# Optimization experiments

Hardware: AMD Instinct MI355X
Metric: run time of the kernel (lower is better)

Reference implementation:

```python
import jax, jax.numpy as jnp
import numpy as np
from jax import lax


def T_grid(t, num_coeff):
    # Chebyshev polynomials T_0..T_{N-1} evaluated at t -> (N, len(t))
    rows = [jnp.ones_like(t), t]
    for _ in range(2, num_coeff):
        rows.append(2.0 * t * rows[-1] - rows[-2])
    return jnp.stack(rows[:num_coeff], axis=0)


def setup_inputs() -> dict:
    key = jax.random.key(0)
    k1, k2, k3, k4, k5 = jax.random.split(key, 5)
    B, D, H, N, T = 128, 512, 1024, 32, 16
    return {
        "t_span": jnp.linspace(0.0, 1.0, T, dtype=jnp.float32),
        "y_init": jax.random.normal(k1, (B, D), dtype=jnp.float32),
        "B_init": jax.random.uniform(k2, (B, D, N), dtype=jnp.float32),
        "W1": jax.random.normal(k3, (D, H), dtype=jnp.float32) / jnp.sqrt(jnp.float32(D)),
        "b1": jax.random.normal(k4, (H,), dtype=jnp.float32),
        "W2": jax.random.normal(k5, (H, D), dtype=jnp.float32) / jnp.sqrt(jnp.float32(H)),
        "num_coeff_per_dim": 32,
        "max_iters": 10,
    }


def reference(t_span, y_init, B_init, W1, b1, W2, num_coeff_per_dim, max_iters):
    N = num_coeff_per_dim
    t0, t1 = t_span[0], t_span[-1]

    # Chebyshev-Gauss-Lobatto nodes on [-1, 1] and Simpson midpoints interleaved
    t_cheb = -jnp.cos(jnp.pi * (jnp.arange(N, dtype=t_span.dtype) / (N - 1)))  # (N,)
    mids = 0.5 * (t_cheb[1:] + t_cheb[:-1])
    t_simpsons = jnp.zeros(2 * N - 1, dtype=t_span.dtype).at[::2].set(t_cheb).at[1::2].set(mids)
    t_true = t0 + 0.5 * (t1 - t0) * (t_simpsons + 1.0)  # (2N-1,)

    Phi_f = T_grid(t_simpsons, N)        # (N, 2N-1)
    Phi = Phi_f[:, ::2]                  # (N, N), invert ONCE (reused every iter)
    Phi_inv = jnp.linalg.inv(Phi)
    widths = (t_true[2::2] - t_true[:-2:2]) / 6.0  # (N-1,) Simpson interval weights

    def f_all(Y):  # vector field f(t, y) = tanh(y @ W1 + t*b1) @ W2, all nodes at once
        # Y: (B, D, M) with M = 2N-1
        h = jnp.tanh(jnp.einsum("bdm,dh->bhm", Y, W1) + t_true[None, None, :] * b1[None, :, None])
        return jnp.einsum("bhm,hd->bdm", h, W2)

    def step(Bc, _):
        approx = jnp.einsum("bdn,nm->bdm", Bc, Phi_f)          # (B, D, 2N-1)
        fap = f_all(approx)
        # Simpson's rule per Chebyshev interval, then cumulative integral S
        s = widths * (fap[..., :-2:2] + 4.0 * fap[..., 1:-1:2] + fap[..., 2::2])  # (B,D,N-1)
        S = jnp.concatenate([jnp.zeros_like(s[..., :1]), jnp.cumsum(s, axis=-1)], axis=-1)
        # torch.linalg.solve(Phi, S + y0, left=False): Bn @ Phi = S + y0
        Bn = (S + y_init[..., None]) @ Phi_inv
        return Bn, None

    B_final, _ = lax.scan(step, B_init, None, length=max_iters)

    t_out = -1.0 + 2.0 * (t_span - t0) / (t1 - t0)
    Phi_out = T_grid(t_out, N)                                  # (N, T)
    approx = jnp.einsum("bdn,nt->bdt", B_final, Phi_out)        # (B, D, T)
    return jnp.moveaxis(approx, -1, 0), B_final                 # (T, B, D), (B, D, N)
```

## Files before the change

### kernel.cpp

```cpp
#include <hip/hip_runtime.h>
#include <hip/hip_bf16.h>
#include <math.h>

#define BB 128
#define DD 512
#define HH 1024
#define NB 32
#define MM 63
#define TT 16
#define ITERS 10

#define OFF_U       0
#define OFF_TTRUE   64
#define OFF_PHIOUT  128
#define OFF_PHIF_BF 1024
#define OFF_QT_BF   2048
#define HDRF        4096
#define OFF_PTPA    HDRF
#define OFF_PTP0    (OFF_PTPA + 2097152)
#define OFF_W1P     (OFF_PTP0 + 2097152)
#define OFF_W2P     (OFF_W1P + 262144)
#define OFF_WWP     (OFF_W2P + 262144)
#define OFF_YW1     (OFF_WWP + 524288)

typedef __attribute__((ext_vector_type(8))) short bf16x8;
typedef __attribute__((ext_vector_type(4))) float f32x4;

static __device__ __forceinline__ unsigned short f2bf(float f) {
    unsigned int x = __builtin_bit_cast(unsigned int, f);
    unsigned int r = x + 0x7FFFu + ((x >> 16) & 1u);
    return (unsigned short)(r >> 16);
}

static __device__ __forceinline__ void store4bf(unsigned short* p,
                                                float v0, float v1, float v2, float v3) {
    unsigned int lo = (unsigned int)f2bf(v0) | ((unsigned int)f2bf(v1) << 16);
    unsigned int hi = (unsigned int)f2bf(v2) | ((unsigned int)f2bf(v3) << 16);
    uint2 u; u.x = lo; u.y = hi;
    *(uint2*)p = u;
}

static __device__ __forceinline__ float tanh_fast(float x) {
    float e = exp2f(x * 2.88539008177793f);
    return 1.0f - 2.0f / (e + 1.0f);
}

static __device__ __forceinline__ unsigned short* aS(unsigned short* smA, int r, int c16) {
    return (unsigned short*)((char*)smA + (((r << 10) + (c16 << 4)) ^ ((r & 7) << 4)));
}

__global__ __launch_bounds__(256) void prologue_kernel(
        const float* __restrict__ t_span, const float* __restrict__ W1,
        const float* __restrict__ W2, const float* __restrict__ y_init,
        float* __restrict__ ws) {
    __shared__ __align__(16) char smem[66560];
    const int bid  = blockIdx.x;
    const int t    = threadIdx.x;
    const int lane = t & 63;
    const int w    = t >> 6;
    const int q    = lane >> 4;
    const int l15  = lane & 15;

    if (bid == 0) {
        double* tsim    = (double*)(smem + 0);
        double* ttrue_d = (double*)(smem + 512);
        double* wid     = (double*)(smem + 1024);
        double* phid    = (double*)(smem + 1280);
        double* pinv    = (double*)(smem + 17408);
        double* Rl      = (double*)(smem + 34048);
        double* Qd      = (double*)(smem + 50176);

        const double PI = 3.14159265358979323846;
        const double t0 = (double)t_span[0];
        const double t1 = (double)t_span[TT - 1];

        if (t < MM) {
            double v;
            if ((t & 1) == 0) {
                int j = t >> 1;
                v = -cos(PI * (double)j / (double)(NB - 1));
            } else {
                int i = t >> 1;
                double a = -cos(PI * (double)i / (double)(NB - 1));
                double b = -cos(PI * (double)(i + 1) / (double)(NB - 1));
                v = 0.5 * (a + b);
            }
            tsim[t] = v;
            ttrue_d[t] = t0 + 0.5 * (t1 - t0) * (v + 1.0);
        }
        __syncthreads();
        if (t < 31) wid[t] = (ttrue_d[2 * t + 2] - ttrue_d[2 * t]) / 6.0;
        if (t < MM) ws[OFF_TTRUE + t] = (float)ttrue_d[t];
        if (t == 63) ws[OFF_TTRUE + 63] = 0.0f;

        if (t < MM) {
            double x = tsim[t];
            double r0 = 1.0, r1 = x;
            phid[0 * MM + t] = r0;
            phid[1 * MM + t] = r1;
            for (int n = 2; n < NB; n++) {
                double r2 = 2.0 * x * r1 - r0;
                phid[n * MM + t] = r2;
                r0 = r1; r1 = r2;
            }
        }

        for (int f = t; f < NB * NB; f += 256) {
            int i = f >> 5, j = f & 31;
            double ci = (i == 0 || i == NB - 1) ? 2.0 : 1.0;
            double cj = (j == 0 || j == NB - 1) ? 2.0 : 1.0;
            double v = 2.0 * cos(PI * (double)(i * j) / (double)(NB - 1))
                       / ((double)(NB - 1) * ci * cj);
            pinv[f] = (j & 1) ? -v : v;
        }
        __syncthreads();

        {
            unsigned short* pf = (unsigned short*)(ws + OFF_PHIF_BF);
            for (int f = t; f < 64 * 32; f += 256) {
                int m = f >> 5, n = f & 31;
                pf[f] = f2bf(m < MM ? (float)phid[n * MM + m] : 0.0f);
            }
        }

        if (t < MM) {
            double acc = 0.0;
            Rl[t * NB + 0] = 0.0;
            for (int i = 1; i < NB; i++) {
                int ip = i - 1;
                double wv = 0.0;
                if (t == 2 * ip)     wv += wid[ip];
                if (t == 2 * ip + 1) wv += 4.0 * wid[ip];
                if (t == 2 * ip + 2) wv += wid[ip];
                acc += wv;
                Rl[t * NB + i] = acc;
            }
        }
        __syncthreads();

        for (int f = t; f < MM * NB; f += 256) {
            int m = f >> 5, j = f & 31;
            double s = 0.0;
            for (int i = 0; i < NB; i++) s += Rl[m * NB + i] * pinv[i * 32 + j];
            Qd[f] = s;
        }
        __syncthreads();

        {
            unsigned short* qt = (unsigned short*)(ws + OFF_QT_BF);
            for (int f = t; f < 32 * 64; f += 256) {
                int j = f >> 6, m = f & 63;
                qt[f] = f2bf(m < MM ? (float)Qd[m * NB + j] : 0.0f);
            }
        }
        if (t < NB) {
            double s = 0.0;
            for (int i = 0; i < NB; i++) s += pinv[i * 32 + t];
            ws[OFF_U + t] = (float)s;
        }
        if (t < TT) {
            double x = -1.0 + 2.0 * ((double)t_span[t] - t0) / (t1 - t0);
            double r0 = 1.0, r1 = x;
            ws[OFF_PHIOUT + 0 * TT + t] = 1.0f;
            ws[OFF_PHIOUT + 1 * TT + t] = (float)x;
            for (int n = 2; n < NB; n++) {
                double r2 = 2.0 * x * r1 - r0;
                ws[OFF_PHIOUT + n * TT + t] = (float)r2;
                r0 = r1; r1 = r2;
            }
        }
        return;
    }

    if (bid <= 64) {
        unsigned short* W1p = (unsigned short*)(ws + OFF_W1P);
        const int hb = bid - 1;
        #pragma unroll
        for (int i = 0; i < 4; i++) {
            int f = i * 256 + t;
            int ds = f >> 6, ln = f & 63;
            int qq = ln >> 4, ll = ln & 15;
            unsigned short tmp[8];
            #pragma unroll
            for (int e = 0; e < 8; e++)
                tmp[e] = f2bf(W1[(size_t)(ds * 32 + qq * 8 + e) * HH + hb * 16 + ll]);
            *(uint4*)(W1p + ((size_t)(hb * 16 + ds) * 64 + ln) * 8) = *(uint4*)tmp;
        }
        return;
    }

    if (bid <= 96) {
        unsigned short* W2p = (unsigned short*)(ws + OFF_W2P);
        const int db = bid - 65;
        #pragma unroll
        for (int i = 0; i < 8; i++) {
            int f = i * 256 + t;
            int hs = f >> 6, ln = f & 63;
            int qq = ln >> 4, ll = ln & 15;
            unsigned short tmp[8];
            #pragma unroll
            for (int e = 0; e < 8; e++)
                tmp[e] = f2bf(W2[(size_t)(hs * 32 + qq * 8 + e) * DD + db * 16 + ll]);
            *(uint4*)(W2p + ((size_t)(db * 32 + hs) * 64 + ln) * 8) = *(uint4*)tmp;
        }
        return;
    }

    unsigned short* lw1t = (unsigned short*)smem;

    if (bid <= 352) {
        unsigned short* WWp = (unsigned short*)(ws + OFF_WWP);
        unsigned short* pbounce = (unsigned short*)(smem + 33280);
        const int idx   = bid - 97;
        const int h2grp = idx & 31;
        const int hpb   = (idx >> 5) * 4 + w;
        const int h2c0  = h2grp * 32;

        for (int i = 0; i < 64; i++) {
            int f = i * 256 + t;
            int row = f >> 5, col = f & 31;
            lw1t[col * 520 + row] = f2bf(W1[(size_t)row * HH + h2c0 + col]);
        }
        __syncthreads();

        f32x4 acc[2][2] = {};
        #pragma unroll 4
        for (int ds = 0; ds < 16; ds++) {
            bf16x8 a[2];
            #pragma unroll
            for (int mt = 0; mt < 2; mt++) {
                const float* w2r = W2 + (size_t)(hpb * 32 + mt * 16 + l15) * DD + ds * 32 + q * 8;
                float4 va = *(const float4*)w2r;
                float4 vb = *(const float4*)(w2r + 4);
                unsigned short tmp[8] = { f2bf(va.x), f2bf(va.y), f2bf(va.z), f2bf(va.w),
                                          f2bf(vb.x), f2bf(vb.y), f2bf(vb.z), f2bf(vb.w) };
                a[mt] = *(bf16x8*)tmp;
            }
            bf16x8 bb0 = *(const bf16x8*)(lw1t + l15 * 520 + ds * 32 + q * 8);
            bf16x8 bb1 = *(const bf16x8*)(lw1t + (16 + l15) * 520 + ds * 32 + q * 8);
            acc[0][0] = __builtin_amdgcn_mfma_f32_16x16x32_bf16(a[0], bb0, acc[0][0], 0, 0, 0);
            acc[0][1] = __builtin_amdgcn_mfma_f32_16x16x32_bf16(a[0], bb1, acc[0][1], 0, 0, 0);
            acc[1][0] = __builtin_amdgcn_mfma_f32_16x16x32_bf16(a[1], bb0, acc[1][0], 0, 0, 0);
            acc[1][1] = __builtin_amdgcn_mfma_f32_16x16x32_bf16(a[1], bb1, acc[1][1], 0, 0, 0);
        }
        unsigned short* pb = pbounce + w * 1024;
        #pragma unroll
        for (int mt = 0; mt < 2; mt++)
            #pragma unroll
            for (int nt = 0; nt < 2; nt++) {
                int lane8 = (mt * 2 + (q >> 1)) * 16 + l15;
                #pragma unroll
                for (int r = 0; r < 4; r++)
                    pb[(nt * 64 + lane8) * 8 + (q & 1) * 4 + r] = f2bf(acc[mt][nt][r]);
            }
        uint4 f0 = *(uint4*)(pb + (0 * 64 + lane) * 8);
        uint4 f1 = *(uint4*)(pb + (1 * 64 + lane) * 8);
        int h2b0 = h2grp * 2;
        *(uint4*)(WWp + ((size_t)(h2b0 + 0) * 32 + hpb) * 512 + lane * 8) = f0;
        *(uint4*)(WWp + ((size_t)(h2b0 + 1) * 32 + hpb) * 512 + lane * 8) = f1;
        return;
    }

    {
        float* yW1 = ws + OFF_YW1;
        const int h2grp = bid - 353;
        const int h2c0  = h2grp * 32;

        for (int i = 0; i < 64; i++) {
            int f = i * 256 + t;
            int row = f >> 5, col = f & 31;
            lw1t[col * 520 + row] = f2bf(W1[(size_t)row * HH + h2c0 + col]);
        }
        __syncthreads();

        f32x4 acc[2][2] = {};
        #pragma unroll 4
        for (int ds = 0; ds < 16; ds++) {
            bf16x8 a[2];
            #pragma unroll
            for (int mt = 0; mt < 2; mt++) {
                const float* yr = y_init + (size_t)(w * 32 + mt * 16 + l15) * DD + ds * 32 + q * 8;
                float4 va = *(const float4*)yr;
                float4 vb = *(const float4*)(yr + 4);
                unsigned short tmp[8] = { f2bf(va.x), f2bf(va.y), f2bf(va.z), f2bf(va.w),
                                          f2bf(vb.x), f2bf(vb.y), f2bf(vb.z), f2bf(vb.w) };
                a[mt] = *(bf16x8*)tmp;
            }
            bf16x8 bb0 = *(const bf16x8*)(lw1t + l15 * 520 + ds * 32 + q * 8);
            bf16x8 bb1 = *(const bf16x8*)(lw1t + (16 + l15) * 520 + ds * 32 + q * 8);
            acc[0][0] = __builtin_amdgcn_mfma_f32_16x16x32_bf16(a[0], bb0, acc[0][0], 0, 0, 0);
            acc[0][1] = __builtin_amdgcn_mfma_f32_16x16x32_bf16(a[0], bb1, acc[0][1], 0, 0, 0);
            acc[1][0] = __builtin_amdgcn_mfma_f32_16x16x32_bf16(a[1], bb0, acc[1][0], 0, 0, 0);
            acc[1][1] = __builtin_amdgcn_mfma_f32_16x16x32_bf16(a[1], bb1, acc[1][1], 0, 0, 0);
        }
        #pragma unroll
        for (int mt = 0; mt < 2; mt++)
            #pragma unroll
            for (int nt = 0; nt < 2; nt++)
                #pragma unroll
                for (int r = 0; r < 4; r++) {
                    int b  = w * 32 + mt * 16 + q * 4 + r;
                    int h2 = h2c0 + nt * 16 + l15;
                    yW1[(size_t)b * HH + h2] = acc[mt][nt][r];
                }
    }
}

__global__ __launch_bounds__(256) void k1_kernel(
        const float* __restrict__ B_init,
        const unsigned short* __restrict__ W1p,
        const float* __restrict__ b1,
        const float* __restrict__ ws,
        unsigned short* __restrict__ Ptp)
{
    __shared__ __align__(16) char smem[40960];
    unsigned short* smA  = (unsigned short*)smem;
    unsigned short* t_sb = (unsigned short*)smem;
    unsigned short* g_sb = (unsigned short*)(smem + 32768);

    const int t    = threadIdx.x;
    const int lane = t & 63;
    const int w    = t >> 6;
    const int q    = lane >> 4;
    const int l15  = lane & 15;
    const int bid  = blockIdx.x;
    const int b    = bid & 127;
    const int hblk = bid >> 7;
    const int hw   = hblk * 128 + w * 32;

    {
        const float* Bi = B_init + (size_t)b * DD * NB;
        #pragma unroll 8
        for (int i = 0; i < 64; i++) {
            int f = i * 256 + t;
            int d = f >> 5, n = f & 31;
            *(unsigned short*)(smem + (((n << 10) + (d << 1)) ^ ((n & 7) << 4)))
                = f2bf(Bi[f]);
        }
    }
    __syncthreads();

    f32x4 acc[2][2] = {};
    const unsigned short* W1b = W1p + (size_t)(hw >> 4) * 8192;
    #pragma unroll 4
    for (int d0 = 0; d0 < DD; d0 += 32) {
        int c16 = (d0 >> 3) + q;
        int ds  = d0 >> 5;
        bf16x8 a0  = *(const bf16x8*)aS(smA, l15, c16);
        bf16x8 a1  = *(const bf16x8*)aS(smA, 16 + l15, c16);
        bf16x8 bb0 = *(const bf16x8*)(W1b + ds * 512 + lane * 8);
        bf16x8 bb1 = *(const bf16x8*)(W1b + 8192 + ds * 512 + lane * 8);
        acc[0][0] = __builtin_amdgcn_mfma_f32_16x16x32_bf16(a0, bb0, acc[0][0], 0, 0, 0);
        acc[0][1] = __builtin_amdgcn_mfma_f32_16x16x32_bf16(a0, bb1, acc[0][1], 0, 0, 0);
        acc[1][0] = __builtin_amdgcn_mfma_f32_16x16x32_bf16(a1, bb0, acc[1][0], 0, 0, 0);
        acc[1][1] = __builtin_amdgcn_mfma_f32_16x16x32_bf16(a1, bb1, acc[1][1], 0, 0, 0);
    }
    #pragma unroll
    for (int mt = 0; mt < 2; mt++)
        #pragma unroll
        for (int nt = 0; nt < 2; nt++) {
            int hl = w * 32 + nt * 16 + l15;
            store4bf(&g_sb[hl * 32 + mt * 16 + q * 4],
                     acc[mt][nt][0], acc[mt][nt][1], acc[mt][nt][2], acc[mt][nt][3]);
        }
    __syncthreads();

    f32x4 zacc[4][2] = {};
    const unsigned short* PF = (const unsigned short*)(ws + OFF_PHIF_BF);
    bf16x8 gb[2];
    #pragma unroll
    for (int nt = 0; nt < 2; nt++)
        gb[nt] = *(const bf16x8*)(&g_sb[(w * 32 + nt * 16 + l15) * 32 + q * 8]);
    #pragma unroll
    for (int mt = 0; mt < 4; mt++) {
        bf16x8 af = *(const bf16x8*)(PF + (mt * 16 + l15) * 32 + q * 8);
        zacc[mt][0] = __builtin_amdgcn_mfma_f32_16x16x32_bf16(af, gb[0], zacc[mt][0], 0, 0, 0);
        zacc[mt][1] = __builtin_amdgcn_mfma_f32_16x16x32_bf16(af, gb[1], zacc[mt][1], 0, 0, 0);
    }

    const float* TTp = ws + OFF_TTRUE;
    float b1v[2] = { b1[hw + l15], b1[hw + 16 + l15] };
    #pragma unroll
    for (int mt = 0; mt < 4; mt++) {
        float4 ttv = *(const float4*)(TTp + mt * 16 + q * 4);
        #pragma unroll
        for (int nt = 0; nt < 2; nt++) {
            int hl = w * 32 + nt * 16 + l15;
            float v0 = tanh_fast(zacc[mt][nt][0] + ttv.x * b1v[nt]);
            float v1 = tanh_fast(zacc[mt][nt][1] + ttv.y * b1v[nt]);
            float v2 = tanh_fast(zacc[mt][nt][2] + ttv.z * b1v[nt]);
            float v3 = tanh_fast(zacc[mt][nt][3] + ttv.w * b1v[nt]);
            store4bf(&t_sb[hl * 72 + mt * 16 + q * 4], v0, v1, v2, v3);
        }
    }
    __syncthreads();

    f32x4 pacc[2][2] = {};
    const unsigned short* QT = (const unsigned short*)(ws + OFF_QT_BF);
    #pragma unroll
    for (int ks = 0; ks < 2; ks++) {
        bf16x8 bt[2];
        #pragma unroll
        for (int nt = 0; nt < 2; nt++)
            bt[nt] = *(const bf16x8*)(&t_sb[(w * 32 + nt * 16 + l15) * 72 + ks * 32 + q * 8]);
        #pragma unroll
        for (int jt = 0; jt < 2; jt++) {
            bf16x8 aq = *(const bf16x8*)(QT + (jt * 16 + l15) * 64 + ks * 32 + q * 8);
            pacc[jt][0] = __builtin_amdgcn_mfma_f32_16x16x32_bf16(aq, bt[0], pacc[jt][0], 0, 0, 0);
            pacc[jt][1] = __builtin_amdgcn_mfma_f32_16x16x32_bf16(aq, bt[1], pacc[jt][1], 0, 0, 0);
        }
    }

    {
        unsigned short* pb = g_sb + w * 1024;
        #pragma unroll
        for (int jt = 0; jt < 2; jt++)
            #pragma unroll
            for (int nt = 0; nt < 2; nt++) {
                int grp = (nt * 2 + (l15 >> 3)) & 3;
                #pragma unroll
                for (int r = 0; r < 4; r++) {
                    int lane8 = grp * 16 + q * 4 + r;
                    pb[(jt * 64 + lane8) * 8 + (l15 & 7)] = f2bf(pacc[jt][nt][r]);
                }
            }
        int hs = hblk * 4 + w;
        uint4 f0 = *(uint4*)(pb + (0 * 64 + lane) * 8);
        uint4 f1 = *(uint4*)(pb + (1 * 64 + lane) * 8);
        *(uint4*)(Ptp + (((size_t)(b * 32 + hs) * 2 + 0) * 64 + lane) * 8) = f0;
        *(uint4*)(Ptp + (((size_t)(b * 32 + hs) * 2 + 1) * 64 + lane) * 8) = f1;
    }
}

__global__ __launch_bounds__(256) void kf_kernel(
        const unsigned short* __restrict__ Ptin,
        const unsigned short* __restrict__ WWp,
        const float* __restrict__ yW1,
        const float* __restrict__ b1,
        const float* __restrict__ ws,
        unsigned short* __restrict__ Ptout)
{
    __shared__ __align__(16) char smem[69632];
    const int t    = threadIdx.x;
    const int lane = t & 63;
    const int w    = t >> 6;
    const int q    = lane >> 4;
    const int l15  = lane & 15;
    const int bid  = blockIdx.x;
    const int b    = bid & 127;
    const int hblk2 = bid >> 7;
    const int hw   = hblk2 * 256 + w * 64;

    f32x4 acc[2][4] = {};
    const unsigned short* Ab  = Ptin + (size_t)b * 32768;
    const unsigned short* WWb = WWp + (size_t)(hblk2 * 16 + w * 4) * 16384;
    unsigned short* buf0 = (unsigned short*)smem;
    unsigned short* buf1 = (unsigned short*)(smem + 16384);

    {
        const uint4* src = (const uint4*)Ab;
        uint4* dst = (uint4*)buf0;
        #pragma unroll
        for (int i = 0; i < 4; i++) dst[i * 256 + t] = src[i * 256 + t];
    }
    __syncthreads();

    #pragma unroll 1
    for (int c = 0; c < 4; ++c) {
        if (c < 3) {
            const uint4* src = (const uint4*)(Ab + (c + 1) * 8192);
            uint4* dst = (uint4*)((c & 1) ? buf0 : buf1);
            #pragma unroll
            for (int i = 0; i < 4; i++) dst[i * 256 + t] = src[i * 256 + t];
        }
        const unsigned short* Ac = (c & 1) ? buf1 : buf0;
        #pragma unroll
        for (int sl = 0; sl < 8; ++sl) {
            int s = c * 8 + sl;
            bf16x8 a0 = *(const bf16x8*)(Ac + (sl * 2 + 0) * 512 + lane * 8);
            bf16x8 a1 = *(const bf16x8*)(Ac + (sl * 2 + 1) * 512 + lane * 8);
            #pragma unroll
            for (int nt = 0; nt < 4; nt++) {
                bf16x8 bb = *(const bf16x8*)(WWb + nt * 16384 + s * 512 + lane * 8);
                acc[0][nt] = __builtin_amdgcn_mfma_f32_16x16x32_bf16(a0, bb, acc[0][nt], 0, 0, 0);
                acc[1][nt] = __builtin_amdgcn_mfma_f32_16x16x32_bf16(a1, bb, acc[1][nt], 0, 0, 0);
            }
        }
        __syncthreads();
    }

    unsigned short* g_w  = (unsigned short*)(smem + w * 4096);
    unsigned short* t_w  = (unsigned short*)(smem + 16384 + w * 9216);
    unsigned short* pb_w = (unsigned short*)(smem + 53248 + w * 4096);

    const float* U = ws + OFF_U;
    float yw[4];
    #pragma unroll
    for (int nt = 0; nt < 4; nt++)
        yw[nt] = yW1[(size_t)b * HH + hw + nt * 16 + l15];
    #pragma unroll
    for (int mt = 0; mt < 2; mt++) {
        float4 uv = *(const float4*)(U + mt * 16 + q * 4);
        #pragma unroll
        for (int nt = 0; nt < 4; nt++) {
            int hl = nt * 16 + l15;
            store4bf(&g_w[hl * 32 + mt * 16 + q * 4],
                     acc[mt][nt][0] + uv.x * yw[nt],
                     acc[mt][nt][1] + uv.y * yw[nt],
                     acc[mt][nt][2] + uv.z * yw[nt],
                     acc[mt][nt][3] + uv.w * yw[nt]);
        }
    }

    f32x4 zacc[4][4] = {};
    const unsigned short* PF = (const unsigned short*)(ws + OFF_PHIF_BF);
    bf16x8 gb[4];
    #pragma unroll
    for (int nt = 0; nt < 4; nt++)
        gb[nt] = *(const bf16x8*)(&g_w[(nt * 16 + l15) * 32 + q * 8]);
    #pragma unroll
    for (int mt = 0; mt < 4; mt++) {
        bf16x8 af = *(const bf16x8*)(PF + (mt * 16 + l15) * 32 + q * 8);
        #pragma unroll
        for (int nt = 0; nt < 4; nt++)
            zacc[mt][nt] = __builtin_amdgcn_mfma_f32_16x16x32_bf16(af, gb[nt], zacc[mt][nt], 0, 0, 0);
    }

    const float* TTp = ws + OFF_TTRUE;
    float b1v[4];
    #pragma unroll
    for (int nt = 0; nt < 4; nt++)
        b1v[nt] = b1[hw + nt * 16 + l15];
    #pragma unroll
    for (int mt = 0; mt < 4; mt++) {
        float4 ttv = *(const float4*)(TTp + mt * 16 + q * 4);
        #pragma unroll
        for (int nt = 0; nt < 4; nt++) {
            int hl = nt * 16 + l15;
            float v0 = tanh_fast(zacc[mt][nt][0] + ttv.x * b1v[nt]);
            float v1 = tanh_fast(zacc[mt][nt][1] + ttv.y * b1v[nt]);
            float v2 = tanh_fast(zacc[mt][nt][2] + ttv.z * b1v[nt]);
            float v3 = tanh_fast(zacc[mt][nt][3] + ttv.w * b1v[nt]);
            store4bf(&t_w[hl * 72 + mt * 16 + q * 4], v0, v1, v2, v3);
        }
    }

    f32x4 pacc[2][4] = {};
    const unsigned short* QT = (const unsigned short*)(ws + OFF_QT_BF);
    #pragma unroll
    for (int ks = 0; ks < 2; ks++) {
        bf16x8 bt[4];
        #pragma unroll
        for (int nt = 0; nt < 4; nt++)
            bt[nt] = *(const bf16x8*)(&t_w[(nt * 16 + l15) * 72 + ks * 32 + q * 8]);
        #pragma unroll
        for (int jt = 0; jt < 2; jt++) {
            bf16x8 aq = *(const bf16x8*)(QT + (jt * 16 + l15) * 64 + ks * 32 + q * 8);
            #pragma unroll
            for (int nt = 0; nt < 4; nt++)
                pacc[jt][nt] = __builtin_amdgcn_mfma_f32_16x16x32_bf16(aq, bt[nt], pacc[jt][nt], 0, 0, 0);
        }
    }

    {
        #pragma unroll
        for (int jt = 0; jt < 2; jt++)
            #pragma unroll
            for (int nt = 0; nt < 4; nt++) {
                int grp    = ((nt & 1) * 2 + (l15 >> 3)) & 3;
                int hs_loc = nt >> 1;
                #pragma unroll
                for (int r = 0; r < 4; r++) {
                    int lane8 = grp * 16 + q * 4 + r;
                    pb_w[(hs_loc * 2 + jt) * 512 + lane8 * 8 + (l15 & 7)] = f2bf(pacc[jt][nt][r]);
                }
            }
        int hs0 = hblk2 * 8 + w * 2;
        #pragma unroll
        for (int i = 0; i < 4; i++) {
            uint4 fv = *(uint4*)(pb_w + i * 512 + lane * 8);
            int hs = hs0 + (i >> 1), jt = i & 1;
            *(uint4*)(Ptout + (((size_t)(b * 32 + hs) * 2 + jt) * 64 + lane) * 8) = fv;
        }
    }
}

__global__ __launch_bounds__(256) void k2f_kernel(
        const unsigned short* __restrict__ Ptp,
        const unsigned short* __restrict__ W2p,
        const float* __restrict__ y_init,
        const float* __restrict__ ws,
        float* __restrict__ out)
{
    __shared__ __align__(16) float ls[4 * 544];
    __shared__ float phiout_s[NB * TT];

    const int t    = threadIdx.x;
    const int lane = t & 63;
    const int w    = t >> 6;
    const int q    = lane >> 4;
    const int l15  = lane & 15;
    const int bid  = blockIdx.x;
    const int b    = bid & 127;
    const int dblk = bid >> 7;
    const int dw   = dblk * 64 + w * 16;

    for (int f = t; f < NB * TT; f += 256) phiout_s[f] = ws[OFF_PHIOUT + f];

    f32x4 acc[2] = {};
    const unsigned short* Ab  = Ptp + (size_t)b * 32768;
    const unsigned short* W2b = W2p + (size_t)(dblk * 4 + w) * 16384;
    #pragma unroll 4
    for (int s = 0; s < 32; s++) {
        bf16x8 a0 = *(const bf16x8*)(Ab + (s * 2 + 0) * 512 + lane * 8);
        bf16x8 a1 = *(const bf16x8*)(Ab + (s * 2 + 1) * 512 + lane * 8);
        bf16x8 bb = *(const bf16x8*)(W2b + s * 512 + lane * 8);
        acc[0] = __builtin_amdgcn_mfma_f32_16x16x32_bf16(a0, bb, acc[0], 0, 0, 0);
        acc[1] = __builtin_amdgcn_mfma_f32_16x16x32_bf16(a1, bb, acc[1], 0, 0, 0);
    }

    const float* U = ws + OFF_U;
    float yv = y_init[(size_t)b * DD + dw + l15];
    #pragma unroll
    for (int mt = 0; mt < 2; mt++) {
        float4 uv = *(const float4*)(U + mt * 16 + q * 4);
        #pragma unroll
        for (int r = 0; r < 4; r++) {
            int j = mt * 16 + q * 4 + r;
            float uvr = (r == 0) ? uv.x : (r == 1) ? uv.y : (r == 2) ? uv.z : uv.w;
            ls[w * 544 + j * 17 + l15] = acc[mt][r] + yv * uvr;
        }
    }
    __syncthreads();

    float* out1 = out + (size_t)TT * BB * DD;
    #pragma unroll
    for (int it = 0; it < 8; it++) {
        int f = it * 64 + lane;
        int d_l = f >> 5, j2 = f & 31;
        out1[((size_t)b * DD + dw + d_l) * NB + j2] = ls[w * 544 + j2 * 17 + d_l];
    }

    #pragma unroll
    for (int i = 0; i < 4; i++) {
        int idx = i * 256 + t;
        int t16 = idx >> 6, dl = idx & 63;
        float s = 0.f;
        #pragma unroll
        for (int n = 0; n < NB; n++)
            s += ls[(dl >> 4) * 544 + n * 17 + (dl & 15)] * phiout_s[n * TT + t16];
        out[(size_t)t16 * (BB * DD) + (size_t)b * DD + dblk * 64 + dl] = s;
    }
}

extern "C" void kernel_launch(void* const* d_in, const int* in_sizes, int n_in,
                              void* d_out, int out_size, void* d_ws, size_t ws_size,
                              hipStream_t stream) {
    const float* t_span = (const float*)d_in[0];
    const float* y_init = (const float*)d_in[1];
    const float* B_init = (const float*)d_in[2];
    const float* W1     = (const float*)d_in[3];
    const float* b1     = (const float*)d_in[4];
    const float* W2     = (const float*)d_in[5];
    float* ws  = (float*)d_ws;
    float* out = (float*)d_out;

    unsigned short* W1p  = (unsigned short*)(ws + OFF_W1P);
    unsigned short* W2p  = (unsigned short*)(ws + OFF_W2P);
    unsigned short* WWp  = (unsigned short*)(ws + OFF_WWP);
    float*          yW1  = ws + OFF_YW1;
    unsigned short* PtpA = (unsigned short*)(ws + OFF_PTPA);
    unsigned short* PtpB = (unsigned short*)(ws + OFF_PTP0);

    prologue_kernel<<<dim3(385), 256, 0, stream>>>(t_span, W1, W2, y_init, ws);

    k1_kernel<<<dim3(1024), 256, 0, stream>>>(B_init, W1p, b1, ws, PtpA);

    unsigned short* pin  = PtpA;
    unsigned short* pout = PtpB;
    for (int it = 1; it < ITERS; it++) {
        kf_kernel<<<dim3(512), 256, 0, stream>>>(pin, WWp, yW1, b1, ws, pout);
        unsigned short* tmp = pin; pin = pout; pout = tmp;
    }
    k2f_kernel<<<dim3(1024), 256, 0, stream>>>(pin, W2p, y_init, ws, out);
}
```

Before: 338.4 us.

## Halve per-block H tile in kf_kernel and double grid to 1024 blocks

Each block of the fused iteration kernel now covers 128 hidden units instead of 256, with each wave handling 32 instead of 64. The grid grows from 512 to 1024 blocks, shared memory drops from 68 KB to 32 KB, and the accumulator arrays shrink. The aim is more parallelism and occupancy on the GPU's many CUs. In exchange, each block's A-tile (Ptin per batch row) is loaded from global memory twice as often, so there is less reuse per load.

```diff
diff --git a/kernel.cpp b/kernel.cpp
--- a/kernel.cpp
+++ b/kernel.cpp
@@ -440,7 +440,7 @@
         const float* __restrict__ ws,
         unsigned short* __restrict__ Ptout)
 {
-    __shared__ __align__(16) char smem[69632];
+    __shared__ __align__(16) char smem[32768];
     const int t    = threadIdx.x;
     const int lane = t & 63;
     const int w    = t >> 6;
@@ -448,12 +448,12 @@
     const int l15  = lane & 15;
     const int bid  = blockIdx.x;
     const int b    = bid & 127;
-    const int hblk2 = bid >> 7;
-    const int hw   = hblk2 * 256 + w * 64;
-
-    f32x4 acc[2][4] = {};
+    const int hblk = bid >> 7;
+    const int hw   = hblk * 128 + w * 32;
+
+    f32x4 acc[2][2] = {};
     const unsigned short* Ab  = Ptin + (size_t)b * 32768;
-    const unsigned short* WWb = WWp + (size_t)(hblk2 * 16 + w * 4) * 16384;
+    const unsigned short* WWb = WWp + (size_t)(hw >> 4) * 16384;
     unsigned short* buf0 = (unsigned short*)smem;
     unsigned short* buf1 = (unsigned short*)(smem + 16384);
 
@@ -477,32 +477,29 @@
         #pragma unroll
         for (int sl = 0; sl < 8; ++sl) {
             int s = c * 8 + sl;
-            bf16x8 a0 = *(const bf16x8*)(Ac + (sl * 2 + 0) * 512 + lane * 8);
-            bf16x8 a1 = *(const bf16x8*)(Ac + (sl * 2 + 1) * 512 + lane * 8);
-            #pragma unroll
-            for (int nt = 0; nt < 4; nt++) {
-                bf16x8 bb = *(const bf16x8*)(WWb + nt * 16384 + s * 512 + lane * 8);
-                acc[0][nt] = __builtin_amdgcn_mfma_f32_16x16x32_bf16(a0, bb, acc[0][nt], 0, 0, 0);
-                acc[1][nt] = __builtin_amdgcn_mfma_f32_16x16x32_bf16(a1, bb, acc[1][nt], 0, 0, 0);
-            }
+            bf16x8 a0  = *(const bf16x8*)(Ac + (sl * 2 + 0) * 512 + lane * 8);
+            bf16x8 a1  = *(const bf16x8*)(Ac + (sl * 2 + 1) * 512 + lane * 8);
+            bf16x8 bb0 = *(const bf16x8*)(WWb + s * 512 + lane * 8);
+            bf16x8 bb1 = *(const bf16x8*)(WWb + 16384 + s * 512 + lane * 8);
+            acc[0][0] = __builtin_amdgcn_mfma_f32_16x16x32_bf16(a0, bb0, acc[0][0], 0, 0, 0);
+            acc[0][1] = __builtin_amdgcn_mfma_f32_16x16x32_bf16(a0, bb1, acc[0][1], 0, 0, 0);
+            acc[1][0] = __builtin_amdgcn_mfma_f32_16x16x32_bf16(a1, bb0, acc[1][0], 0, 0, 0);
+            acc[1][1] = __builtin_amdgcn_mfma_f32_16x16x32_bf16(a1, bb1, acc[1][1], 0, 0, 0);
         }
         __syncthreads();
     }
-
-    unsigned short* g_w  = (unsigned short*)(smem + w * 4096);
-    unsigned short* t_w  = (unsigned short*)(smem + 16384 + w * 9216);
-    unsigned short* pb_w = (unsigned short*)(smem + 53248 + w * 4096);
+    unsigned short* g_w = (unsigned short*)(smem + w * 2048);
+    unsigned short* t_w = (unsigned short*)(smem + 8192 + w * 4608);
+    unsigned short* pb_w = g_w;
 
     const float* U = ws + OFF_U;
-    float yw[4];
-    #pragma unroll
-    for (int nt = 0; nt < 4; nt++)
-        yw[nt] = yW1[(size_t)b * HH + hw + nt * 16 + l15];
+    float yw[2] = { yW1[(size_t)b * HH + hw + l15],
+                    yW1[(size_t)b * HH + hw + 16 + l15] };
     #pragma unroll
     for (int mt = 0; mt < 2; mt++) {
         float4 uv = *(const float4*)(U + mt * 16 + q * 4);
         #pragma unroll
-        for (int nt = 0; nt < 4; nt++) {
+        for (int nt = 0; nt < 2; nt++) {
             int hl = nt * 16 + l15;
             store4bf(&g_w[hl * 32 + mt * 16 + q * 4],
                      acc[mt][nt][0] + uv.x * yw[nt],
@@ -512,30 +509,26 @@
         }
     }
 
-    f32x4 zacc[4][4] = {};
+    f32x4 zacc[4][2] = {};
     const unsigned short* PF = (const unsigned short*)(ws + OFF_PHIF_BF);
-    bf16x8 gb[4];
-    #pragma unroll
-    for (int nt = 0; nt < 4; nt++)
+    bf16x8 gb[2];
+    #pragma unroll
+    for (int nt = 0; nt < 2; nt++)
         gb[nt] = *(const bf16x8*)(&g_w[(nt * 16 + l15) * 32 + q * 8]);
     #pragma unroll
     for (int mt = 0; mt < 4; mt++) {
         bf16x8 af = *(const bf16x8*)(PF + (mt * 16 + l15) * 32 + q * 8);
-        #pragma unroll
-        for (int nt = 0; nt < 4; nt++)
-            zacc[mt][nt] = __builtin_amdgcn_mfma_f32_16x16x32_bf16(af, gb[nt], zacc[mt][nt], 0, 0, 0);
+        zacc[mt][0] = __builtin_amdgcn_mfma_f32_16x16x32_bf16(af, gb[0], zacc[mt][0], 0, 0, 0);
+        zacc[mt][1] = __builtin_amdgcn_mfma_f32_16x16x32_bf16(af, gb[1], zacc[mt][1], 0, 0, 0);
     }
 
     const float* TTp = ws + OFF_TTRUE;
-    float b1v[4];
-    #pragma unroll
-    for (int nt = 0; nt < 4; nt++)
-        b1v[nt] = b1[hw + nt * 16 + l15];
+    float b1v[2] = { b1[hw + l15], b1[hw + 16 + l15] };
     #pragma unroll
     for (int mt = 0; mt < 4; mt++) {
         float4 ttv = *(const float4*)(TTp + mt * 16 + q * 4);
         #pragma unroll
-        for (int nt = 0; nt < 4; nt++) {
+        for (int nt = 0; nt < 2; nt++) {
             int hl = nt * 16 + l15;
             float v0 = tanh_fast(zacc[mt][nt][0] + ttv.x * b1v[nt]);
             float v1 = tanh_fast(zacc[mt][nt][1] + ttv.y * b1v[nt]);
@@ -545,20 +538,19 @@
         }
     }
 
-    f32x4 pacc[2][4] = {};
+    f32x4 pacc[2][2] = {};
     const unsigned short* QT = (const unsigned short*)(ws + OFF_QT_BF);
     #pragma unroll
     for (int ks = 0; ks < 2; ks++) {
-        bf16x8 bt[4];
-        #pragma unroll
-        for (int nt = 0; nt < 4; nt++)
+        bf16x8 bt[2];
+        #pragma unroll
+        for (int nt = 0; nt < 2; nt++)
             bt[nt] = *(const bf16x8*)(&t_w[(nt * 16 + l15) * 72 + ks * 32 + q * 8]);
         #pragma unroll
         for (int jt = 0; jt < 2; jt++) {
             bf16x8 aq = *(const bf16x8*)(QT + (jt * 16 + l15) * 64 + ks * 32 + q * 8);
-            #pragma unroll
-            for (int nt = 0; nt < 4; nt++)
-                pacc[jt][nt] = __builtin_amdgcn_mfma_f32_16x16x32_bf16(aq, bt[nt], pacc[jt][nt], 0, 0, 0);
+            pacc[jt][0] = __builtin_amdgcn_mfma_f32_16x16x32_bf16(aq, bt[0], pacc[jt][0], 0, 0, 0);
+            pacc[jt][1] = __builtin_amdgcn_mfma_f32_16x16x32_bf16(aq, bt[1], pacc[jt][1], 0, 0, 0);
         }
     }
 
@@ -566,22 +558,19 @@
         #pragma unroll
         for (int jt = 0; jt < 2; jt++)
             #pragma unroll
-            for (int nt = 0; nt < 4; nt++) {
-                int grp    = ((nt & 1) * 2 + (l15 >> 3)) & 3;
-                int hs_loc = nt >> 1;
+            for (int nt = 0; nt < 2; nt++) {
+                int grp = (nt * 2 + (l15 >> 3)) & 3;
                 #pragma unroll
                 for (int r = 0; r < 4; r++) {
                     int lane8 = grp * 16 + q * 4 + r;
-                    pb_w[(hs_loc * 2 + jt) * 512 + lane8 * 8 + (l15 & 7)] = f2bf(pacc[jt][nt][r]);
+                    pb_w[(jt * 64 + lane8) * 8 + (l15 & 7)] = f2bf(pacc[jt][nt][r]);
                 }
             }
-        int hs0 = hblk2 * 8 + w * 2;
-        #pragma unroll
-        for (int i = 0; i < 4; i++) {
-            uint4 fv = *(uint4*)(pb_w + i * 512 + lane * 8);
-            int hs = hs0 + (i >> 1), jt = i & 1;
-            *(uint4*)(Ptout + (((size_t)(b * 32 + hs) * 2 + jt) * 64 + lane) * 8) = fv;
-        }
+        int hs = hblk * 4 + w;
+        uint4 f0 = *(uint4*)(pb_w + (0 * 64 + lane) * 8);
+        uint4 f1 = *(uint4*)(pb_w + (1 * 64 + lane) * 8);
+        *(uint4*)(Ptout + (((size_t)(b * 32 + hs) * 2 + 0) * 64 + lane) * 8) = f0;
+        *(uint4*)(Ptout + (((size_t)(b * 32 + hs) * 2 + 1) * 64 + lane) * 8) = f1;
     }
 }
 
@@ -679,7 +668,7 @@
     unsigned short* pin  = PtpA;
     unsigned short* pout = PtpB;
     for (int it = 1; it < ITERS; it++) {
-        kf_kernel<<<dim3(512), 256, 0, stream>>>(pin, WWp, yW1, b1, ws, pout);
+        kf_kernel<<<dim3(1024), 256, 0, stream>>>(pin, WWp, yW1, b1, ws, pout);
         unsigned short* tmp = pin; pin = pout; pout = tmp;
     }
     k2f_kernel<<<dim3(1024), 256, 0, stream>>>(pin, W2p, y_init, ws, out);
```

New measurement: 318.9 us (median of 2 runs). -5.8%, faster.
